# Optimization experiments

Hardware: AMD Instinct MI355X
Metric: run time of the kernel (lower is better)

## Reference

```python
import jax, jax.numpy as jnp
import numpy as np

B, T, N, F = 32, 256, 68, 64
NUM_LAYERS = 3
EPS = 1e-5


def _build_adjacency(n):
    a = np.zeros((n, n), dtype=np.float32)
    i = np.arange(n)
    a[i[1:], i[1:] - 1] = 1.0
    a[i[:-1], i[:-1] + 1] = 1.0
    return jnp.asarray(a)


def setup_inputs() -> dict:
    key = jax.random.key(0)
    ks = jax.random.split(key, 10)
    x = jax.random.normal(ks[0], (B, T, N, 2), dtype=jnp.float32)
    adj = _build_adjacency(N)  # (N, N) tridiagonal buffer (not trainable)
    W_enc = jax.random.normal(ks[1], (2, F), dtype=jnp.float32) * 0.5
    b_enc = jax.random.normal(ks[2], (F,), dtype=jnp.float32) * 0.05
    W_gnn = jax.random.normal(ks[3], (NUM_LAYERS, F, F), dtype=jnp.float32) * (1.0 / np.sqrt(F))
    b_gnn = jax.random.normal(ks[4], (NUM_LAYERS, F), dtype=jnp.float32) * 0.05
    gamma = jnp.ones((NUM_LAYERS, F), dtype=jnp.float32)
    beta = jnp.zeros((NUM_LAYERS, F), dtype=jnp.float32)
    W1 = jax.random.normal(ks[5], (F, 32), dtype=jnp.float32) * (1.0 / np.sqrt(F))
    b1 = jax.random.normal(ks[6], (32,), dtype=jnp.float32) * 0.05
    W2 = jax.random.normal(ks[7], (32, 1), dtype=jnp.float32) * (1.0 / np.sqrt(32))
    b2 = jax.random.normal(ks[8], (1,), dtype=jnp.float32) * 0.05
    return {"landmarks_sequence": x, "adj": adj, "W_enc": W_enc, "b_enc": b_enc,
            "W_gnn": W_gnn, "b_gnn": b_gnn, "gamma": gamma, "beta": beta,
            "W1": W1, "b1": b1, "W2": W2, "b2": b2}


def _layernorm(z, g, b):
    mu = jnp.mean(z, axis=-1, keepdims=True)
    var = jnp.mean(jnp.square(z - mu), axis=-1, keepdims=True)
    return (z - mu) * jax.lax.rsqrt(var + EPS) * g + b


def reference(landmarks_sequence, adj, W_enc, b_enc, W_gnn, b_gnn, gamma, beta, W1, b1, W2, b2):
    # Vectorize the torch per-timestep Python loop: all T timesteps at once.
    # node encoder: (B,T,N,2) -> (B,T,N,F)
    h = landmarks_sequence @ W_enc + b_enc
    for l in range(NUM_LAYERS):
        # neighbor aggregation via tridiagonal adjacency (same math as dense NxN matmul)
        agg = jnp.einsum('nm,btmf->btnf', adj, h)
        z = jax.nn.relu(agg @ W_gnn[l] + b_gnn[l])
        h = _layernorm(z, gamma[l], beta[l]) + h  # residual
    pooled = jnp.mean(h, axis=2)                  # AdaptiveAvgPool1d(1) over nodes -> (B,T,F)
    logits = jax.nn.relu(pooled @ W1 + b1) @ W2 + b2  # (B,T,1)
    return jnp.mean(logits, axis=1).squeeze(-1)       # mean over T, squeeze -> (B,)
```

## Files before the change

kernel.cpp:

```cpp
#include <hip/hip_runtime.h>

#define B_SZ 32
#define T_SZ 256
#define N_NODES 68
#define NLAYERS 3
#define EPS 1e-5f

#define HP 72
#define HROWS 70

typedef _Float16 f16x8 __attribute__((ext_vector_type(8)));
typedef _Float16 f16x4 __attribute__((ext_vector_type(4)));
typedef _Float16 f16x2 __attribute__((ext_vector_type(2)));
typedef __fp16   fp16v2 __attribute__((ext_vector_type(2)));
typedef float    f32x4 __attribute__((ext_vector_type(4)));
typedef int      v2i   __attribute__((ext_vector_type(2)));

__device__ __forceinline__ float red16(float x) {
#if __has_builtin(__builtin_amdgcn_permlane16_swap)
    v2i r = __builtin_amdgcn_permlane16_swap(__float_as_int(x), __float_as_int(x),
                                             false, false);
    return __int_as_float(r[0]) + __int_as_float(r[1]);
#else
    return x + __shfl_xor(x, 16);
#endif
}
__device__ __forceinline__ float red32(float x) {
#if __has_builtin(__builtin_amdgcn_permlane32_swap)
    v2i r = __builtin_amdgcn_permlane32_swap(__float_as_int(x), __float_as_int(x),
                                             false, false);
    return __int_as_float(r[0]) + __int_as_float(r[1]);
#else
    return x + __shfl_xor(x, 32);
#endif
}

__device__ __forceinline__ f16x2 pack2(float a, float b) {
    fp16v2 p = __builtin_amdgcn_cvt_pkrtz(a, b);
    return __builtin_bit_cast(f16x2, p);
}
__device__ __forceinline__ f16x4 pack4(float a, float b, float c, float d) {
    f16x2 lo = pack2(a, b);
    f16x2 hi = pack2(c, d);
    f16x4 o;
    o[0] = lo[0]; o[1] = lo[1]; o[2] = hi[0]; o[3] = hi[1];
    return o;
}

__global__ void prep_k(const float* __restrict__ W, const float* __restrict__ W1,
                       const float* __restrict__ gamma, const float* __restrict__ beta,
                       _Float16* __restrict__ Wt, float* __restrict__ W1t,
                       _Float16* __restrict__ gb16, float* __restrict__ out) {
    int idx = blockIdx.x * 256 + threadIdx.x;
    if (idx < 12288) {
        int l = idx >> 12, r = idx & 4095;
        int m = r >> 6, k = r & 63;
        Wt[(l << 12) + (m << 6) + k] = (_Float16)W[(l << 12) + (k << 6) + m];
    } else if (idx < 14336) {
        int r = idx - 12288;
        int j = r >> 6, f = r & 63;
        W1t[r] = W1[f * 32 + j];
    } else if (idx < 14720) {
        int r = idx - 14336;
        gb16[r] = (_Float16)(r < 192 ? gamma[r] : beta[r - 192]);
    } else if (idx < 14752) {
        out[idx - 14720] = 0.f;
    }
}

__global__ __launch_bounds__(256, 2)
void gnn_wave(const float* __restrict__ x,
              const float* __restrict__ W_enc, const float* __restrict__ b_enc,
              const _Float16* __restrict__ Wt, const float* __restrict__ b_gnn,
              const _Float16* __restrict__ gb16,
              const float* __restrict__ W1t, const float* __restrict__ b1,
              const float* __restrict__ W2, const float* __restrict__ b2,
              float* __restrict__ out)
{
    __shared__ _Float16 hsh[4][HROWS * HP];

    const int tid  = threadIdx.x;
    const int lane = tid & 63;
    const int wave = tid >> 6;
    const int l15  = lane & 15;
    const int quad = lane >> 4;

    _Float16* h = hsh[wave];
    const int g = blockIdx.x * 4 + wave;
    const float* xp = x + (size_t)g * (N_NODES * 2);

    if (lane < 36) {
        ((unsigned*)h)[lane] = 0u;
        ((unsigned*)(h + 69 * HP))[lane] = 0u;
    }

    {
        float2 xr[17];
        #pragma unroll
        for (int i = 0; i < 17; ++i)
            xr[i] = *(const float2*)&xp[(i * 4 + quad) * 2];

        const f32x4 we0 = ((const f32x4*)W_enc)[l15];
        const f32x4 we1 = ((const f32x4*)(W_enc + 64))[l15];
        const f32x4 be  = ((const f32x4*)b_enc)[l15];
        #pragma unroll
        for (int i = 0; i < 17; ++i) {
            int n = i * 4 + quad;
            f32x4 hv = xr[i].x * we0 + xr[i].y * we1 + be;
            *(f16x4*)&h[(n + 1) * HP + l15 * 4] = pack4(hv[0], hv[1], hv[2], hv[3]);
        }
    }

    #pragma unroll 1
    for (int l = 0; l < NLAYERS; ++l) {
        const _Float16* WtL = Wt + (l << 12);

        __builtin_amdgcn_sched_barrier(0);

        f16x8 a0[4], a1[4];
        f32x4 bgv[4];
        f16x4 gmv[4], bbv[4];
        #pragma unroll
        for (int s = 0; s < 4; ++s) {
            a0[s]  = *(const f16x8*)&WtL[(s * 16 + l15) * 64 + quad * 8];
            a1[s]  = *(const f16x8*)&WtL[(s * 16 + l15) * 64 + 32 + quad * 8];
            bgv[s] = *(const f32x4*)&b_gnn[l * 64 + s * 16 + quad * 4];
            gmv[s] = *(const f16x4*)&gb16[l * 64 + s * 16 + quad * 4];
            bbv[s] = *(const f16x4*)&gb16[192 + l * 64 + s * 16 + quad * 4];
        }

        f16x8 ra0, ra1, rc0, rc1, na0, na1, nc0, nc1;
        {
            const _Float16* hb = h + l15 * HP + quad * 8;
            ra0 = *(const f16x8*)hb;            ra1 = *(const f16x8*)(hb + 32);
            rc0 = *(const f16x8*)(hb + 2 * HP); rc1 = *(const f16x8*)(hb + 2 * HP + 32);
        }

        #pragma unroll
        for (int t = 0; t < 5; ++t) {
            if (t < 4) {
                int n  = (t + 1) * 16 + l15;
                int nc = (t == 3) ? (n > 67 ? 67 : n) : n;
                const _Float16* hb = h + nc * HP + quad * 8;
                na0 = *(const f16x8*)hb;            na1 = *(const f16x8*)(hb + 32);
                nc0 = *(const f16x8*)(hb + 2 * HP); nc1 = *(const f16x8*)(hb + 2 * HP + 32);
            }
            const int rn = t * 16 + l15 + 1;
            f16x4 hv[4];
            #pragma unroll
            for (int s = 0; s < 4; ++s)
                hv[s] = *(const f16x4*)&h[rn * HP + s * 16 + quad * 4];

            f16x8 bc0 = ra0 + rc0;
            f16x8 bc1 = ra1 + rc1;

            f32x4 acc[4];
            #pragma unroll
            for (int s = 0; s < 4; ++s) {
                f32x4 z = bgv[s];
                z = __builtin_amdgcn_mfma_f32_16x16x32_f16(a0[s], bc0, z, 0, 0, 0);
                z = __builtin_amdgcn_mfma_f32_16x16x32_f16(a1[s], bc1, z, 0, 0, 0);
                acc[s] = z;
            }

            float Sp[4], Qp[4];
            #pragma unroll
            for (int s = 0; s < 4; ++s) {
                f32x4 zz = acc[s];
                float s0 = 0.f, q0 = 0.f;
                #pragma unroll
                for (int i = 0; i < 4; ++i) {
                    float zv = fmaxf(zz[i], 0.f);
                    zz[i] = zv; s0 += zv; q0 = fmaf(zv, zv, q0);
                }
                Sp[s] = s0; Qp[s] = q0;
                acc[s] = zz;
            }
            float S = (Sp[0] + Sp[1]) + (Sp[2] + Sp[3]);
            float Q = (Qp[0] + Qp[1]) + (Qp[2] + Qp[3]);
            S = red16(S); Q = red16(Q);
            S = red32(S); Q = red32(Q);
            const float mu = S * (1.f / 64.f);
            const float rs = rsqrtf(fmaf(-mu, mu, Q * (1.f / 64.f)) + EPS);
            const float m2 = -mu * rs;

            __builtin_amdgcn_sched_barrier(0x47F);

            if (t < 4 || l15 < 4) {
                #pragma unroll
                for (int s = 0; s < 4; ++s) {
                    f16x4 th = pack4(fmaf(acc[s][0], rs, m2), fmaf(acc[s][1], rs, m2),
                                     fmaf(acc[s][2], rs, m2), fmaf(acc[s][3], rs, m2));
                    f16x4 r = th * gmv[s] + bbv[s] + hv[s];
                    *(f16x4*)&h[rn * HP + s * 16 + quad * 4] = r;
                }
            }

            ra0 = na0; ra1 = na1; rc0 = nc0; rc1 = nc1;
        }
    }

    __builtin_amdgcn_sched_barrier(0);

    f32x4 pp[4] = {{0.f,0.f,0.f,0.f},{0.f,0.f,0.f,0.f},
                   {0.f,0.f,0.f,0.f},{0.f,0.f,0.f,0.f}};
    #pragma unroll
    for (int i = 0; i < 17; ++i) {
        f16x4 hv = *(const f16x4*)&h[(i * 4 + quad + 1) * HP + l15 * 4];
        f32x4 a = {(float)hv[0], (float)hv[1], (float)hv[2], (float)hv[3]};
        pp[i & 3] += a;
    }
    f32x4 ps = (pp[0] + pp[1]) + (pp[2] + pp[3]);
    #pragma unroll
    for (int i = 0; i < 4; ++i)
        ps[i] = red32(red16(ps[i])) * (1.f / (float)N_NODES);

    __builtin_amdgcn_sched_barrier(0x47F);
    float* scr = (float*)h;
    if (quad == 0) *(f32x4*)&scr[l15 * 4] = ps;
    __builtin_amdgcn_sched_barrier(0x47F);

    {
        const int j = lane & 31, hf = lane >> 5;
        float a = hf ? 0.f : b1[j];
        const float* wrow = W1t + j * 64 + hf * 32;
        const float* pvp  = scr + hf * 32;
        #pragma unroll
        for (int k = 0; k < 8; ++k) {
            f32x4 pw = *(const f32x4*)&wrow[k * 4];
            f32x4 pv = *(const f32x4*)&pvp[k * 4];
            a = fmaf(pv[0], pw[0], a); a = fmaf(pv[1], pw[1], a);
            a = fmaf(pv[2], pw[2], a); a = fmaf(pv[3], pw[3], a);
        }
        float full = red32(a);
        float v = fmaxf(full, 0.f) * W2[j];
        v += __shfl_xor(v, 16);
        v += __shfl_xor(v, 8);
        v += __shfl_xor(v, 4);
        v += __shfl_xor(v, 2);
        v += __shfl_xor(v, 1);
        if (lane == 0)
            atomicAdd(out + (g >> 8), (v + b2[0]) * (1.f / (float)T_SZ));
    }
}

extern "C" void kernel_launch(void* const* d_in, const int* in_sizes, int n_in,
                              void* d_out, int out_size, void* d_ws, size_t ws_size,
                              hipStream_t stream) {
    const float* x     = (const float*)d_in[0];
    const float* W_enc = (const float*)d_in[2];
    const float* b_enc = (const float*)d_in[3];
    const float* W_gnn = (const float*)d_in[4];
    const float* b_gnn = (const float*)d_in[5];
    const float* gamma = (const float*)d_in[6];
    const float* beta  = (const float*)d_in[7];
    const float* W1    = (const float*)d_in[8];
    const float* b1    = (const float*)d_in[9];
    const float* W2    = (const float*)d_in[10];
    const float* b2    = (const float*)d_in[11];
    float* out = (float*)d_out;

    _Float16* Wt   = (_Float16*)d_ws;
    float*    W1t  = (float*)((char*)d_ws + (1 << 15));
    _Float16* gb16 = (_Float16*)((char*)d_ws + 49152);

    prep_k<<<58, 256, 0, stream>>>(W_gnn, W1, gamma, beta, Wt, W1t, gb16, out);

    const int n_graphs = B_SZ * T_SZ;
    gnn_wave<<<n_graphs / 4, 256, 0, stream>>>(x, W_enc, b_enc, Wt, b_gnn,
                                               gb16, W1t, b1, W2, b2, out);
}
```

Baseline: 178.8 us.

## Process two graphs per wave to share weight fragments and interleave MFMA chains

Each wave now handles two graphs instead of one. The block shrinks to 128 threads while keeping four graphs per block. The per-layer weight, bias and LayerNorm fragments loaded into registers are reused across both graphs, and the two independent MFMA and reduction chains are interleaved to hide latency. The neighbor prefetch is restructured so only one row is carried across iterations and the other is loaded in the same iteration. The final MLP is merged into a single reduction with a doubled b2 term. Register pressure rises, which could reduce occupancy, and there are half as many waves to hide latency.

```diff
diff --git a/kernel.cpp b/kernel.cpp
--- a/kernel.cpp
+++ b/kernel.cpp
@@ -68,7 +68,7 @@
     }
 }
 
-__global__ __launch_bounds__(256, 2)
+__global__ __launch_bounds__(128, 2)
 void gnn_wave(const float* __restrict__ x,
               const float* __restrict__ W_enc, const float* __restrict__ b_enc,
               const _Float16* __restrict__ Wt, const float* __restrict__ b_gnn,
@@ -85,29 +85,32 @@
     const int l15  = lane & 15;
     const int quad = lane >> 4;
 
-    _Float16* h = hsh[wave];
-    const int g = blockIdx.x * 4 + wave;
-    const float* xp = x + (size_t)g * (N_NODES * 2);
+    _Float16* h0 = hsh[wave * 2 + 0];
+    _Float16* h1 = hsh[wave * 2 + 1];
+    const int g0 = blockIdx.x * 4 + wave * 2;
+    const float* xp0 = x + (size_t)g0 * (N_NODES * 2);
+    const float* xp1 = xp0 + (N_NODES * 2);
 
     if (lane < 36) {
-        ((unsigned*)h)[lane] = 0u;
-        ((unsigned*)(h + 69 * HP))[lane] = 0u;
+        ((unsigned*)h0)[lane] = 0u;
+        ((unsigned*)(h0 + 69 * HP))[lane] = 0u;
+        ((unsigned*)h1)[lane] = 0u;
+        ((unsigned*)(h1 + 69 * HP))[lane] = 0u;
     }
 
     {
-        float2 xr[17];
-        #pragma unroll
-        for (int i = 0; i < 17; ++i)
-            xr[i] = *(const float2*)&xp[(i * 4 + quad) * 2];
-
         const f32x4 we0 = ((const f32x4*)W_enc)[l15];
         const f32x4 we1 = ((const f32x4*)(W_enc + 64))[l15];
         const f32x4 be  = ((const f32x4*)b_enc)[l15];
         #pragma unroll
         for (int i = 0; i < 17; ++i) {
             int n = i * 4 + quad;
-            f32x4 hv = xr[i].x * we0 + xr[i].y * we1 + be;
-            *(f16x4*)&h[(n + 1) * HP + l15 * 4] = pack4(hv[0], hv[1], hv[2], hv[3]);
+            float2 xa = *(const float2*)&xp0[n * 2];
+            float2 xb = *(const float2*)&xp1[n * 2];
+            f32x4 ha = xa.x * we0 + xa.y * we1 + be;
+            f32x4 hb = xb.x * we0 + xb.y * we1 + be;
+            *(f16x4*)&h0[(n + 1) * HP + l15 * 4] = pack4(ha[0], ha[1], ha[2], ha[3]);
+            *(f16x4*)&h1[(n + 1) * HP + l15 * 4] = pack4(hb[0], hb[1], hb[2], hb[3]);
         }
     }
 
@@ -129,118 +132,153 @@
             bbv[s] = *(const f16x4*)&gb16[192 + l * 64 + s * 16 + quad * 4];
         }
 
-        f16x8 ra0, ra1, rc0, rc1, na0, na1, nc0, nc1;
+        f16x8 xA0, xA1, yA0, yA1, nxA0, nxA1, nyA0, nyA1;
         {
-            const _Float16* hb = h + l15 * HP + quad * 8;
-            ra0 = *(const f16x8*)hb;            ra1 = *(const f16x8*)(hb + 32);
-            rc0 = *(const f16x8*)(hb + 2 * HP); rc1 = *(const f16x8*)(hb + 2 * HP + 32);
+            const _Float16* q0 = h0 + l15 * HP + quad * 8;
+            const _Float16* q1 = h1 + l15 * HP + quad * 8;
+            xA0 = *(const f16x8*)q0; xA1 = *(const f16x8*)(q0 + 32);
+            yA0 = *(const f16x8*)q1; yA1 = *(const f16x8*)(q1 + 32);
         }
 
         #pragma unroll
         for (int t = 0; t < 5; ++t) {
+            const int n  = t * 16 + l15;
+            const int nc = (t == 4) ? (n > 67 ? 67 : n) : n;
+            const int rc = nc + 1;
+
+            const _Float16* p0 = h0 + nc * HP + quad * 8;
+            const _Float16* p1 = h1 + nc * HP + quad * 8;
+            f16x8 C0 = *(const f16x8*)(p0 + 2 * HP), C1 = *(const f16x8*)(p0 + 2 * HP + 32);
+            f16x8 E0 = *(const f16x8*)(p1 + 2 * HP), E1 = *(const f16x8*)(p1 + 2 * HP + 32);
+            f16x4 hv0[4], hv1[4];
+            #pragma unroll
+            for (int s = 0; s < 4; ++s) {
+                hv0[s] = *(const f16x4*)&h0[rc * HP + s * 16 + quad * 4];
+                hv1[s] = *(const f16x4*)&h1[rc * HP + s * 16 + quad * 4];
+            }
             if (t < 4) {
-                int n  = (t + 1) * 16 + l15;
-                int nc = (t == 3) ? (n > 67 ? 67 : n) : n;
-                const _Float16* hb = h + nc * HP + quad * 8;
-                na0 = *(const f16x8*)hb;            na1 = *(const f16x8*)(hb + 32);
-                nc0 = *(const f16x8*)(hb + 2 * HP); nc1 = *(const f16x8*)(hb + 2 * HP + 32);
-            }
-            const int rn = t * 16 + l15 + 1;
-            f16x4 hv[4];
-            #pragma unroll
-            for (int s = 0; s < 4; ++s)
-                hv[s] = *(const f16x4*)&h[rn * HP + s * 16 + quad * 4];
-
-            f16x8 bc0 = ra0 + rc0;
-            f16x8 bc1 = ra1 + rc1;
-
-            f32x4 acc[4];
+                int nn  = (t + 1) * 16 + l15;
+                int nnc = (t == 3) ? (nn > 67 ? 67 : nn) : nn;
+                const _Float16* q0 = h0 + nnc * HP + quad * 8;
+                const _Float16* q1 = h1 + nnc * HP + quad * 8;
+                nxA0 = *(const f16x8*)q0; nxA1 = *(const f16x8*)(q0 + 32);
+                nyA0 = *(const f16x8*)q1; nyA1 = *(const f16x8*)(q1 + 32);
+            }
+
+            f16x8 b00 = xA0 + C0, b01 = xA1 + C1;
+            f16x8 b10 = yA0 + E0, b11 = yA1 + E1;
+            f32x4 acc0[4], acc1[4];
             #pragma unroll
             for (int s = 0; s < 4; ++s) {
                 f32x4 z = bgv[s];
-                z = __builtin_amdgcn_mfma_f32_16x16x32_f16(a0[s], bc0, z, 0, 0, 0);
-                z = __builtin_amdgcn_mfma_f32_16x16x32_f16(a1[s], bc1, z, 0, 0, 0);
-                acc[s] = z;
-            }
-
-            float Sp[4], Qp[4];
+                z = __builtin_amdgcn_mfma_f32_16x16x32_f16(a0[s], b00, z, 0, 0, 0);
+                z = __builtin_amdgcn_mfma_f32_16x16x32_f16(a1[s], b01, z, 0, 0, 0);
+                acc0[s] = z;
+                f32x4 y = bgv[s];
+                y = __builtin_amdgcn_mfma_f32_16x16x32_f16(a0[s], b10, y, 0, 0, 0);
+                y = __builtin_amdgcn_mfma_f32_16x16x32_f16(a1[s], b11, y, 0, 0, 0);
+                acc1[s] = y;
+            }
+
+            float S0 = 0.f, Q0 = 0.f, S1 = 0.f, Q1 = 0.f;
             #pragma unroll
             for (int s = 0; s < 4; ++s) {
-                f32x4 zz = acc[s];
-                float s0 = 0.f, q0 = 0.f;
+                f32x4 za = acc0[s], zb = acc1[s];
                 #pragma unroll
                 for (int i = 0; i < 4; ++i) {
-                    float zv = fmaxf(zz[i], 0.f);
-                    zz[i] = zv; s0 += zv; q0 = fmaf(zv, zv, q0);
+                    float va = fmaxf(za[i], 0.f);
+                    za[i] = va; S0 += va; Q0 = fmaf(va, va, Q0);
+                    float vb = fmaxf(zb[i], 0.f);
+                    zb[i] = vb; S1 += vb; Q1 = fmaf(vb, vb, Q1);
                 }
-                Sp[s] = s0; Qp[s] = q0;
-                acc[s] = zz;
-            }
-            float S = (Sp[0] + Sp[1]) + (Sp[2] + Sp[3]);
-            float Q = (Qp[0] + Qp[1]) + (Qp[2] + Qp[3]);
-            S = red16(S); Q = red16(Q);
-            S = red32(S); Q = red32(Q);
-            const float mu = S * (1.f / 64.f);
-            const float rs = rsqrtf(fmaf(-mu, mu, Q * (1.f / 64.f)) + EPS);
-            const float m2 = -mu * rs;
+                acc0[s] = za; acc1[s] = zb;
+            }
+            S0 = red16(S0); Q0 = red16(Q0); S1 = red16(S1); Q1 = red16(Q1);
+            S0 = red32(S0); Q0 = red32(Q0); S1 = red32(S1); Q1 = red32(Q1);
+            const float mu0 = S0 * (1.f / 64.f);
+            const float rs0 = rsqrtf(fmaf(-mu0, mu0, Q0 * (1.f / 64.f)) + EPS);
+            const float m20 = -mu0 * rs0;
+            const float mu1 = S1 * (1.f / 64.f);
+            const float rs1 = rsqrtf(fmaf(-mu1, mu1, Q1 * (1.f / 64.f)) + EPS);
+            const float m21 = -mu1 * rs1;
 
             __builtin_amdgcn_sched_barrier(0x47F);
 
             if (t < 4 || l15 < 4) {
                 #pragma unroll
                 for (int s = 0; s < 4; ++s) {
-                    f16x4 th = pack4(fmaf(acc[s][0], rs, m2), fmaf(acc[s][1], rs, m2),
-                                     fmaf(acc[s][2], rs, m2), fmaf(acc[s][3], rs, m2));
-                    f16x4 r = th * gmv[s] + bbv[s] + hv[s];
-                    *(f16x4*)&h[rn * HP + s * 16 + quad * 4] = r;
+                    f16x4 ta = pack4(fmaf(acc0[s][0], rs0, m20), fmaf(acc0[s][1], rs0, m20),
+                                     fmaf(acc0[s][2], rs0, m20), fmaf(acc0[s][3], rs0, m20));
+                    f16x4 ra = ta * gmv[s] + bbv[s] + hv0[s];
+                    *(f16x4*)&h0[rc * HP + s * 16 + quad * 4] = ra;
+                    f16x4 tb = pack4(fmaf(acc1[s][0], rs1, m21), fmaf(acc1[s][1], rs1, m21),
+                                     fmaf(acc1[s][2], rs1, m21), fmaf(acc1[s][3], rs1, m21));
+                    f16x4 rb = tb * gmv[s] + bbv[s] + hv1[s];
+                    *(f16x4*)&h1[rc * HP + s * 16 + quad * 4] = rb;
                 }
             }
 
-            ra0 = na0; ra1 = na1; rc0 = nc0; rc1 = nc1;
+            xA0 = nxA0; xA1 = nxA1; yA0 = nyA0; yA1 = nyA1;
         }
     }
 
     __builtin_amdgcn_sched_barrier(0);
 
-    f32x4 pp[4] = {{0.f,0.f,0.f,0.f},{0.f,0.f,0.f,0.f},
+    f32x4 pa[4] = {{0.f,0.f,0.f,0.f},{0.f,0.f,0.f,0.f},
+                   {0.f,0.f,0.f,0.f},{0.f,0.f,0.f,0.f}};
+    f32x4 pb[4] = {{0.f,0.f,0.f,0.f},{0.f,0.f,0.f,0.f},
                    {0.f,0.f,0.f,0.f},{0.f,0.f,0.f,0.f}};
     #pragma unroll
     for (int i = 0; i < 17; ++i) {
-        f16x4 hv = *(const f16x4*)&h[(i * 4 + quad + 1) * HP + l15 * 4];
-        f32x4 a = {(float)hv[0], (float)hv[1], (float)hv[2], (float)hv[3]};
-        pp[i & 3] += a;
-    }
-    f32x4 ps = (pp[0] + pp[1]) + (pp[2] + pp[3]);
+        const int off = (i * 4 + quad + 1) * HP + l15 * 4;
+        f16x4 va = *(const f16x4*)&h0[off];
+        f16x4 vb = *(const f16x4*)&h1[off];
+        pa[i & 3] += (f32x4){(float)va[0], (float)va[1], (float)va[2], (float)va[3]};
+        pb[i & 3] += (f32x4){(float)vb[0], (float)vb[1], (float)vb[2], (float)vb[3]};
+    }
+    f32x4 psa = (pa[0] + pa[1]) + (pa[2] + pa[3]);
+    f32x4 psb = (pb[0] + pb[1]) + (pb[2] + pb[3]);
     #pragma unroll
-    for (int i = 0; i < 4; ++i)
-        ps[i] = red32(red16(ps[i])) * (1.f / (float)N_NODES);
+    for (int i = 0; i < 4; ++i) {
+        psa[i] = red32(red16(psa[i])) * (1.f / (float)N_NODES);
+        psb[i] = red32(red16(psb[i])) * (1.f / (float)N_NODES);
+    }
 
     __builtin_amdgcn_sched_barrier(0x47F);
-    float* scr = (float*)h;
-    if (quad == 0) *(f32x4*)&scr[l15 * 4] = ps;
+    float* scr0 = (float*)h0;
+    float* scr1 = (float*)h1;
+    if (quad == 0) {
+        *(f32x4*)&scr0[l15 * 4] = psa;
+        *(f32x4*)&scr1[l15 * 4] = psb;
+    }
     __builtin_amdgcn_sched_barrier(0x47F);
 
     {
         const int j = lane & 31, hf = lane >> 5;
-        float a = hf ? 0.f : b1[j];
+        const float b1j = hf ? 0.f : b1[j];
+        float aa = b1j, ab = b1j;
         const float* wrow = W1t + j * 64 + hf * 32;
-        const float* pvp  = scr + hf * 32;
         #pragma unroll
         for (int k = 0; k < 8; ++k) {
             f32x4 pw = *(const f32x4*)&wrow[k * 4];
-            f32x4 pv = *(const f32x4*)&pvp[k * 4];
-            a = fmaf(pv[0], pw[0], a); a = fmaf(pv[1], pw[1], a);
-            a = fmaf(pv[2], pw[2], a); a = fmaf(pv[3], pw[3], a);
-        }
-        float full = red32(a);
-        float v = fmaxf(full, 0.f) * W2[j];
+            f32x4 v0 = *(const f32x4*)&scr0[hf * 32 + k * 4];
+            f32x4 v1 = *(const f32x4*)&scr1[hf * 32 + k * 4];
+            aa = fmaf(v0[0], pw[0], aa); aa = fmaf(v0[1], pw[1], aa);
+            aa = fmaf(v0[2], pw[2], aa); aa = fmaf(v0[3], pw[3], aa);
+            ab = fmaf(v1[0], pw[0], ab); ab = fmaf(v1[1], pw[1], ab);
+            ab = fmaf(v1[2], pw[2], ab); ab = fmaf(v1[3], pw[3], ab);
+        }
+        const float w2j = W2[j];
+        float va = fmaxf(red32(aa), 0.f) * w2j;
+        float vb = fmaxf(red32(ab), 0.f) * w2j;
+        float v = va + vb;
         v += __shfl_xor(v, 16);
         v += __shfl_xor(v, 8);
         v += __shfl_xor(v, 4);
         v += __shfl_xor(v, 2);
         v += __shfl_xor(v, 1);
         if (lane == 0)
-            atomicAdd(out + (g >> 8), (v + b2[0]) * (1.f / (float)T_SZ));
+            atomicAdd(out + (g0 >> 8), (v + 2.f * b2[0]) * (1.f / (float)T_SZ));
     }
 }
 
@@ -267,6 +305,6 @@
     prep_k<<<58, 256, 0, stream>>>(W_gnn, W1, gamma, beta, Wt, W1t, gb16, out);
 
     const int n_graphs = B_SZ * T_SZ;
-    gnn_wave<<<n_graphs / 4, 256, 0, stream>>>(x, W_enc, b_enc, Wt, b_gnn,
+    gnn_wave<<<n_graphs / 4, 128, 0, stream>>>(x, W_enc, b_enc, Wt, b_gnn,
                                                gb16, W1t, b1, W2, b2, out);
 }
```

Result: faster. 152.5 us (-14.7%).

## Process four graphs per single-wave block to share weight loads and interleave MFMAs

Applied to the files above, without the earlier changes.

The kernel moves from four waves per block, each handling one graph, to one 64-thread wave handling four graphs at once. Per-layer weights, bias and LayerNorm parameters are loaded once and reused across the four graphs, and their independent MFMA chains and reductions are interleaved to expose ILP. The four pooled contributions are summed and written with a single atomic. The cost is much higher register pressure and fewer waves per block (launch bounds 64,1), which can cut occupancy and latency hiding.

```diff
diff --git a/kernel.cpp b/kernel.cpp
--- a/kernel.cpp
+++ b/kernel.cpp
@@ -8,6 +8,7 @@
 
 #define HP 72
 #define HROWS 70
+#define NS 4
 
 typedef _Float16 f16x8 __attribute__((ext_vector_type(8)));
 typedef _Float16 f16x4 __attribute__((ext_vector_type(4)));
@@ -68,7 +69,7 @@
     }
 }
 
-__global__ __launch_bounds__(256, 2)
+__global__ __launch_bounds__(64, 1)
 void gnn_wave(const float* __restrict__ x,
               const float* __restrict__ W_enc, const float* __restrict__ b_enc,
               const _Float16* __restrict__ Wt, const float* __restrict__ b_gnn,
@@ -77,37 +78,43 @@
               const float* __restrict__ W2, const float* __restrict__ b2,
               float* __restrict__ out)
 {
-    __shared__ _Float16 hsh[4][HROWS * HP];
-
-    const int tid  = threadIdx.x;
-    const int lane = tid & 63;
-    const int wave = tid >> 6;
+    __shared__ _Float16 hsh[NS][HROWS * HP];
+
+    const int lane = threadIdx.x;
     const int l15  = lane & 15;
     const int quad = lane >> 4;
 
-    _Float16* h = hsh[wave];
-    const int g = blockIdx.x * 4 + wave;
-    const float* xp = x + (size_t)g * (N_NODES * 2);
+    const int g0 = blockIdx.x * NS;
+    _Float16* hS[NS];
+    const float* xpS[NS];
+    #pragma unroll
+    for (int s = 0; s < NS; ++s) {
+        hS[s]  = hsh[s];
+        xpS[s] = x + (size_t)(g0 + s) * (N_NODES * 2);
+    }
 
     if (lane < 36) {
-        ((unsigned*)h)[lane] = 0u;
-        ((unsigned*)(h + 69 * HP))[lane] = 0u;
+        #pragma unroll
+        for (int s = 0; s < NS; ++s) {
+            ((unsigned*)hS[s])[lane] = 0u;
+            ((unsigned*)(hS[s] + 69 * HP))[lane] = 0u;
+        }
     }
 
     {
-        float2 xr[17];
-        #pragma unroll
-        for (int i = 0; i < 17; ++i)
-            xr[i] = *(const float2*)&xp[(i * 4 + quad) * 2];
-
         const f32x4 we0 = ((const f32x4*)W_enc)[l15];
         const f32x4 we1 = ((const f32x4*)(W_enc + 64))[l15];
         const f32x4 be  = ((const f32x4*)b_enc)[l15];
         #pragma unroll
         for (int i = 0; i < 17; ++i) {
             int n = i * 4 + quad;
-            f32x4 hv = xr[i].x * we0 + xr[i].y * we1 + be;
-            *(f16x4*)&h[(n + 1) * HP + l15 * 4] = pack4(hv[0], hv[1], hv[2], hv[3]);
+            #pragma unroll
+            for (int s = 0; s < NS; ++s) {
+                float2 xv = *(const float2*)&xpS[s][n * 2];
+                f32x4 hv = xv.x * we0 + xv.y * we1 + be;
+                *(f16x4*)&hS[s][(n + 1) * HP + l15 * 4] =
+                    pack4(hv[0], hv[1], hv[2], hv[3]);
+            }
         }
     }
 
@@ -121,126 +128,172 @@
         f32x4 bgv[4];
         f16x4 gmv[4], bbv[4];
         #pragma unroll
-        for (int s = 0; s < 4; ++s) {
-            a0[s]  = *(const f16x8*)&WtL[(s * 16 + l15) * 64 + quad * 8];
-            a1[s]  = *(const f16x8*)&WtL[(s * 16 + l15) * 64 + 32 + quad * 8];
-            bgv[s] = *(const f32x4*)&b_gnn[l * 64 + s * 16 + quad * 4];
-            gmv[s] = *(const f16x4*)&gb16[l * 64 + s * 16 + quad * 4];
-            bbv[s] = *(const f16x4*)&gb16[192 + l * 64 + s * 16 + quad * 4];
-        }
-
-        f16x8 ra0, ra1, rc0, rc1, na0, na1, nc0, nc1;
-        {
-            const _Float16* hb = h + l15 * HP + quad * 8;
-            ra0 = *(const f16x8*)hb;            ra1 = *(const f16x8*)(hb + 32);
-            rc0 = *(const f16x8*)(hb + 2 * HP); rc1 = *(const f16x8*)(hb + 2 * HP + 32);
+        for (int k = 0; k < 4; ++k) {
+            a0[k]  = *(const f16x8*)&WtL[(k * 16 + l15) * 64 + quad * 8];
+            a1[k]  = *(const f16x8*)&WtL[(k * 16 + l15) * 64 + 32 + quad * 8];
+            bgv[k] = *(const f32x4*)&b_gnn[l * 64 + k * 16 + quad * 4];
+            gmv[k] = *(const f16x4*)&gb16[l * 64 + k * 16 + quad * 4];
+            bbv[k] = *(const f16x4*)&gb16[192 + l * 64 + k * 16 + quad * 4];
+        }
+
+        f16x8 cA0[NS], cA1[NS], nA0[NS], nA1[NS];
+        #pragma unroll
+        for (int s = 0; s < NS; ++s) {
+            const _Float16* q = hS[s] + l15 * HP + quad * 8;
+            cA0[s] = *(const f16x8*)q; cA1[s] = *(const f16x8*)(q + 32);
         }
 
         #pragma unroll
         for (int t = 0; t < 5; ++t) {
+            const int n  = t * 16 + l15;
+            const int nc = (t == 4) ? (n > 67 ? 67 : n) : n;
+            const int rc = nc + 1;
+
+            f16x8 C0[NS], C1[NS];
+            f16x4 hv[NS][4];
+            #pragma unroll
+            for (int s = 0; s < NS; ++s) {
+                const _Float16* p = hS[s] + nc * HP + quad * 8;
+                C0[s] = *(const f16x8*)(p + 2 * HP);
+                C1[s] = *(const f16x8*)(p + 2 * HP + 32);
+                #pragma unroll
+                for (int k = 0; k < 4; ++k)
+                    hv[s][k] = *(const f16x4*)&hS[s][rc * HP + k * 16 + quad * 4];
+            }
             if (t < 4) {
-                int n  = (t + 1) * 16 + l15;
-                int nc = (t == 3) ? (n > 67 ? 67 : n) : n;
-                const _Float16* hb = h + nc * HP + quad * 8;
-                na0 = *(const f16x8*)hb;            na1 = *(const f16x8*)(hb + 32);
-                nc0 = *(const f16x8*)(hb + 2 * HP); nc1 = *(const f16x8*)(hb + 2 * HP + 32);
-            }
-            const int rn = t * 16 + l15 + 1;
-            f16x4 hv[4];
-            #pragma unroll
-            for (int s = 0; s < 4; ++s)
-                hv[s] = *(const f16x4*)&h[rn * HP + s * 16 + quad * 4];
-
-            f16x8 bc0 = ra0 + rc0;
-            f16x8 bc1 = ra1 + rc1;
-
-            f32x4 acc[4];
-            #pragma unroll
-            for (int s = 0; s < 4; ++s) {
-                f32x4 z = bgv[s];
-                z = __builtin_amdgcn_mfma_f32_16x16x32_f16(a0[s], bc0, z, 0, 0, 0);
-                z = __builtin_amdgcn_mfma_f32_16x16x32_f16(a1[s], bc1, z, 0, 0, 0);
-                acc[s] = z;
-            }
-
-            float Sp[4], Qp[4];
-            #pragma unroll
-            for (int s = 0; s < 4; ++s) {
-                f32x4 zz = acc[s];
-                float s0 = 0.f, q0 = 0.f;
-                #pragma unroll
-                for (int i = 0; i < 4; ++i) {
-                    float zv = fmaxf(zz[i], 0.f);
-                    zz[i] = zv; s0 += zv; q0 = fmaf(zv, zv, q0);
+                int nn  = (t + 1) * 16 + l15;
+                int nnc = (t == 3) ? (nn > 67 ? 67 : nn) : nn;
+                #pragma unroll
+                for (int s = 0; s < NS; ++s) {
+                    const _Float16* q = hS[s] + nnc * HP + quad * 8;
+                    nA0[s] = *(const f16x8*)q; nA1[s] = *(const f16x8*)(q + 32);
                 }
-                Sp[s] = s0; Qp[s] = q0;
-                acc[s] = zz;
-            }
-            float S = (Sp[0] + Sp[1]) + (Sp[2] + Sp[3]);
-            float Q = (Qp[0] + Qp[1]) + (Qp[2] + Qp[3]);
-            S = red16(S); Q = red16(Q);
-            S = red32(S); Q = red32(Q);
-            const float mu = S * (1.f / 64.f);
-            const float rs = rsqrtf(fmaf(-mu, mu, Q * (1.f / 64.f)) + EPS);
-            const float m2 = -mu * rs;
+            }
+
+            f32x4 acc[NS][4];
+            #pragma unroll
+            for (int s = 0; s < NS; ++s) {
+                f16x8 b0 = cA0[s] + C0[s];
+                f16x8 b1 = cA1[s] + C1[s];
+                #pragma unroll
+                for (int k = 0; k < 4; ++k) {
+                    f32x4 z = bgv[k];
+                    z = __builtin_amdgcn_mfma_f32_16x16x32_f16(a0[k], b0, z, 0, 0, 0);
+                    z = __builtin_amdgcn_mfma_f32_16x16x32_f16(a1[k], b1, z, 0, 0, 0);
+                    acc[s][k] = z;
+                }
+            }
+
+            float S[NS], Q[NS], mu[NS], rs[NS], m2[NS];
+            #pragma unroll
+            for (int s = 0; s < NS; ++s) { S[s] = 0.f; Q[s] = 0.f; }
+            #pragma unroll
+            for (int s = 0; s < NS; ++s) {
+                #pragma unroll
+                for (int k = 0; k < 4; ++k) {
+                    f32x4 z = acc[s][k];
+                    #pragma unroll
+                    for (int i = 0; i < 4; ++i) {
+                        float v = fmaxf(z[i], 0.f);
+                        z[i] = v; S[s] += v; Q[s] = fmaf(v, v, Q[s]);
+                    }
+                    acc[s][k] = z;
+                }
+            }
+            #pragma unroll
+            for (int s = 0; s < NS; ++s) { S[s] = red16(S[s]); Q[s] = red16(Q[s]); }
+            #pragma unroll
+            for (int s = 0; s < NS; ++s) { S[s] = red32(S[s]); Q[s] = red32(Q[s]); }
+            #pragma unroll
+            for (int s = 0; s < NS; ++s) {
+                mu[s] = S[s] * (1.f / 64.f);
+                rs[s] = rsqrtf(fmaf(-mu[s], mu[s], Q[s] * (1.f / 64.f)) + EPS);
+                m2[s] = -mu[s] * rs[s];
+            }
 
             __builtin_amdgcn_sched_barrier(0x47F);
 
             if (t < 4 || l15 < 4) {
                 #pragma unroll
-                for (int s = 0; s < 4; ++s) {
-                    f16x4 th = pack4(fmaf(acc[s][0], rs, m2), fmaf(acc[s][1], rs, m2),
-                                     fmaf(acc[s][2], rs, m2), fmaf(acc[s][3], rs, m2));
-                    f16x4 r = th * gmv[s] + bbv[s] + hv[s];
-                    *(f16x4*)&h[rn * HP + s * 16 + quad * 4] = r;
+                for (int s = 0; s < NS; ++s) {
+                    #pragma unroll
+                    for (int k = 0; k < 4; ++k) {
+                        f16x4 th = pack4(fmaf(acc[s][k][0], rs[s], m2[s]),
+                                         fmaf(acc[s][k][1], rs[s], m2[s]),
+                                         fmaf(acc[s][k][2], rs[s], m2[s]),
+                                         fmaf(acc[s][k][3], rs[s], m2[s]));
+                        f16x4 r = th * gmv[k] + bbv[k] + hv[s][k];
+                        *(f16x4*)&hS[s][rc * HP + k * 16 + quad * 4] = r;
+                    }
                 }
             }
 
-            ra0 = na0; ra1 = na1; rc0 = nc0; rc1 = nc1;
+            #pragma unroll
+            for (int s = 0; s < NS; ++s) { cA0[s] = nA0[s]; cA1[s] = nA1[s]; }
         }
     }
 
     __builtin_amdgcn_sched_barrier(0);
 
-    f32x4 pp[4] = {{0.f,0.f,0.f,0.f},{0.f,0.f,0.f,0.f},
-                   {0.f,0.f,0.f,0.f},{0.f,0.f,0.f,0.f}};
+    f32x4 ps[NS];
     #pragma unroll
-    for (int i = 0; i < 17; ++i) {
-        f16x4 hv = *(const f16x4*)&h[(i * 4 + quad + 1) * HP + l15 * 4];
-        f32x4 a = {(float)hv[0], (float)hv[1], (float)hv[2], (float)hv[3]};
-        pp[i & 3] += a;
-    }
-    f32x4 ps = (pp[0] + pp[1]) + (pp[2] + pp[3]);
+    for (int s = 0; s < NS; ++s) {
+        f32x4 pp0 = {0.f,0.f,0.f,0.f}, pp1 = {0.f,0.f,0.f,0.f};
+        f32x4 pp2 = {0.f,0.f,0.f,0.f}, pp3 = {0.f,0.f,0.f,0.f};
+        #pragma unroll
+        for (int i = 0; i < 17; ++i) {
+            f16x4 v = *(const f16x4*)&hS[s][(i * 4 + quad + 1) * HP + l15 * 4];
+            f32x4 a = {(float)v[0], (float)v[1], (float)v[2], (float)v[3]};
+            if ((i & 3) == 0) pp0 += a;
+            else if ((i & 3) == 1) pp1 += a;
+            else if ((i & 3) == 2) pp2 += a;
+            else pp3 += a;
+        }
+        ps[s] = (pp0 + pp1) + (pp2 + pp3);
+    }
     #pragma unroll
-    for (int i = 0; i < 4; ++i)
-        ps[i] = red32(red16(ps[i])) * (1.f / (float)N_NODES);
+    for (int s = 0; s < NS; ++s)
+        #pragma unroll
+        for (int i = 0; i < 4; ++i)
+            ps[s][i] = red32(red16(ps[s][i])) * (1.f / (float)N_NODES);
 
     __builtin_amdgcn_sched_barrier(0x47F);
-    float* scr = (float*)h;
-    if (quad == 0) *(f32x4*)&scr[l15 * 4] = ps;
+    if (quad == 0) {
+        #pragma unroll
+        for (int s = 0; s < NS; ++s)
+            *(f32x4*)&((float*)hS[s])[l15 * 4] = ps[s];
+    }
     __builtin_amdgcn_sched_barrier(0x47F);
 
     {
         const int j = lane & 31, hf = lane >> 5;
-        float a = hf ? 0.f : b1[j];
+        const float b1j = hf ? 0.f : b1[j];
+        float a[NS];
+        #pragma unroll
+        for (int s = 0; s < NS; ++s) a[s] = b1j;
         const float* wrow = W1t + j * 64 + hf * 32;
-        const float* pvp  = scr + hf * 32;
         #pragma unroll
         for (int k = 0; k < 8; ++k) {
             f32x4 pw = *(const f32x4*)&wrow[k * 4];
-            f32x4 pv = *(const f32x4*)&pvp[k * 4];
-            a = fmaf(pv[0], pw[0], a); a = fmaf(pv[1], pw[1], a);
-            a = fmaf(pv[2], pw[2], a); a = fmaf(pv[3], pw[3], a);
-        }
-        float full = red32(a);
-        float v = fmaxf(full, 0.f) * W2[j];
+            #pragma unroll
+            for (int s = 0; s < NS; ++s) {
+                f32x4 pv = *(const f32x4*)&((float*)hS[s])[hf * 32 + k * 4];
+                a[s] = fmaf(pv[0], pw[0], a[s]); a[s] = fmaf(pv[1], pw[1], a[s]);
+                a[s] = fmaf(pv[2], pw[2], a[s]); a[s] = fmaf(pv[3], pw[3], a[s]);
+            }
+        }
+        const float w2j = W2[j];
+        float v = 0.f;
+        #pragma unroll
+        for (int s = 0; s < NS; ++s)
+            v += fmaxf(red32(a[s]), 0.f) * w2j;
         v += __shfl_xor(v, 16);
         v += __shfl_xor(v, 8);
         v += __shfl_xor(v, 4);
         v += __shfl_xor(v, 2);
         v += __shfl_xor(v, 1);
         if (lane == 0)
-            atomicAdd(out + (g >> 8), (v + b2[0]) * (1.f / (float)T_SZ));
+            atomicAdd(out + (g0 >> 8), (v + (float)NS * b2[0]) * (1.f / (float)T_SZ));
     }
 }
 
@@ -267,6 +320,6 @@
     prep_k<<<58, 256, 0, stream>>>(W_gnn, W1, gamma, beta, Wt, W1t, gb16, out);
 
     const int n_graphs = B_SZ * T_SZ;
-    gnn_wave<<<n_graphs / 4, 256, 0, stream>>>(x, W_enc, b_enc, Wt, b_gnn,
+    gnn_wave<<<n_graphs / NS, 64, 0, stream>>>(x, W_enc, b_enc, Wt, b_gnn,
                                                gb16, W1t, b1, W2, b2, out);
 }
```

Result: faster. 152.7 us (-14.6%).
